# Optimization experiments

Hardware: AMD Instinct MI355X
Metric: run time of the kernel (lower is better)

The kernel has to match this reference:

```python
import jax, jax.numpy as jnp
import numpy as np

B, S, HID = 2, 2048, 1024
HEADS, DHEAD = 16, 64
INNER = HEADS * DHEAD


def setup_inputs() -> dict:
    key = jax.random.key(0)
    ks = jax.random.split(key, 12)
    s = 0.02
    return {
        "query": jax.random.normal(ks[0], (B, S, HID), jnp.float32),
        "key": jax.random.normal(ks[1], (B, S, HID), jnp.float32),
        "value": jax.random.normal(ks[2], (B, S, HID), jnp.float32),
        "mask": jnp.zeros((B, 1, S, S), jnp.float32),
        "position_bias": jax.random.normal(ks[3], (1, HEADS, S, S), jnp.float32),
        "Wq": jax.random.normal(ks[4], (HID, INNER), jnp.float32) * s,
        "bq": jnp.zeros((INNER,), jnp.float32),
        "Wk": jax.random.normal(ks[5], (HID, INNER), jnp.float32) * s,
        "bk": jnp.zeros((INNER,), jnp.float32),
        "Wv": jax.random.normal(ks[6], (HID, INNER), jnp.float32) * s,
        "bv": jnp.zeros((INNER,), jnp.float32),
        "Wo": jax.random.normal(ks[7], (INNER, HID), jnp.float32) * s,
        "bo": jnp.zeros((HID,), jnp.float32),
    }


def reference(query, key, value, mask, position_bias,
              Wq, bq, Wk, bk, Wv, bv, Wo, bo):
    # project and split heads: [B,S,HID] -> [B,HEADS,S,DHEAD]
    def shape(x, W, b):
        return (x @ W + b).reshape(B, S, HEADS, DHEAD).transpose(0, 2, 1, 3)

    q = shape(query, Wq, bq)
    k = shape(key, Wk, bk)
    v = shape(value, Wv, bv)

    scores = jnp.einsum("bhqd,bhkd->bhqk", q, k)
    scores = scores + position_bias          # bias added BEFORE scaling (as in source)
    scores = scores / jnp.sqrt(jnp.float32(DHEAD))
    scores = scores + mask                   # additive mask
    probs = jax.nn.softmax(scores, axis=-1)  # dropout p=0.0 -> identity

    out = jnp.einsum("bhqk,bhkd->bhqd", probs, v)
    out = out.transpose(0, 2, 1, 3).reshape(B, S, INNER)
    return out @ Wo + bo
```

## Files before the change

kernel.cpp:

```cpp
#include <hip/hip_runtime.h>
#include <cstdint>
#include <cstddef>

#define B_SZ      2
#define S_LEN     2048
#define HID_DIM   1024
#define N_HEAD    16
#define D_HEAD    64
#define INNER_DIM 1024

#define C1 0.18033688011112042f
#define C2 1.44269504088896340736f

typedef __attribute__((ext_vector_type(8))) short bf16x8;
typedef __attribute__((ext_vector_type(4))) float f32x4;

__device__ __forceinline__ unsigned short f2bf(float f) {
  unsigned int u = __float_as_uint(f);
  u += 0x7fffu + ((u >> 16) & 1u);
  return (unsigned short)(u >> 16);
}
__device__ __forceinline__ float bf2f(unsigned short u) {
  return __uint_as_float(((unsigned int)u) << 16);
}

__device__ __forceinline__ void gload_lds16(const void* g, void* l) {
  __builtin_amdgcn_global_load_lds((const __attribute__((address_space(1))) void*)g,
                                   (__attribute__((address_space(3))) void*)l,
                                   16, 0, 0);
}

__global__ void cast3_kernel(const float* __restrict__ i0, const float* __restrict__ i1,
                             const float* __restrict__ i2,
                             unsigned short* __restrict__ o0, unsigned short* __restrict__ o1,
                             unsigned short* __restrict__ o2, int n4) {
  int z = blockIdx.y;
  const float* in = (z == 0) ? i0 : (z == 1) ? i1 : i2;
  unsigned short* out = (z == 0) ? o0 : (z == 1) ? o1 : o2;
  int i = blockIdx.x * blockDim.x + threadIdx.x;
  if (i < n4) {
    float4 v = ((const float4*)in)[i];
    ushort4 o;
    o.x = f2bf(v.x); o.y = f2bf(v.y); o.z = f2bf(v.z); o.w = f2bf(v.w);
    ((ushort4*)out)[i] = o;
  }
}

__global__ void transpose_cast_kernel(const float* __restrict__ in,
                                      unsigned short* __restrict__ out,
                                      int rows, int cols) {
  __shared__ float tile[32][33];
  int bx = blockIdx.x * 32;
  int by = blockIdx.y * 32;
  int tx = threadIdx.x & 31;
  int ty = threadIdx.x >> 5;
#pragma unroll
  for (int i = 0; i < 32; i += 8)
    tile[ty + i][tx] = in[(size_t)(by + ty + i) * cols + bx + tx];
  __syncthreads();
#pragma unroll
  for (int i = 0; i < 32; i += 8)
    out[(size_t)(bx + ty + i) * rows + by + tx] = f2bf(tile[tx][ty + i]);
}


__global__ __launch_bounds__(256, 2)
void qkv_gemm_kernel(const unsigned short* __restrict__ Aq,
                     const unsigned short* __restrict__ Ak,
                     const unsigned short* __restrict__ Av,
                     const unsigned short* __restrict__ Wq,
                     const unsigned short* __restrict__ Wk,
                     const unsigned short* __restrict__ Wv,
                     const float* __restrict__ bq,
                     const float* __restrict__ bk,
                     const float* __restrict__ bv,
                     unsigned short* __restrict__ Oq,
                     unsigned short* __restrict__ Ok,
                     unsigned short* __restrict__ Ov) {
  constexpr int K = 1024;
  __shared__ unsigned short Asm[128 * 64];
  __shared__ unsigned short Bsm[64 * 64];

  const int z = blockIdx.z;
  const unsigned short* A  = (z == 0) ? Aq : (z == 1) ? Ak : Av;
  const unsigned short* Bt = (z == 0) ? Wq : (z == 1) ? Wk : Wv;
  const float* bias        = (z == 0) ? bq : (z == 1) ? bk : bv;
  const float scale        = (z == 0) ? C1 : 1.0f;

  const int tid = threadIdx.x;
  const int lane = tid & 63;
  const int w = tid >> 6;
  const int wm = w & 1;
  const int wn = w >> 1;
  const int c = lane & 15;
  const int g = lane >> 4;
  const int m0 = blockIdx.x * 128;
  const int n0 = blockIdx.y * 64;

  f32x4 acc[4][2];
  f32x4 zero = {0.f, 0.f, 0.f, 0.f};
#pragma unroll
  for (int mt = 0; mt < 4; ++mt)
#pragma unroll
    for (int nt = 0; nt < 2; ++nt) acc[mt][nt] = zero;

  for (int kk = 0; kk < K / 64; ++kk) {
    __syncthreads();
    const int k0 = kk * 64;
#pragma unroll
    for (int it = 0; it < 4; ++it) {
      int slot = it * 256 + tid;
      int r = slot >> 3, sp = slot & 7, seg = sp ^ (r & 7);
      gload_lds16(A + (size_t)(m0 + r) * K + k0 + seg * 8,
                  (char*)Asm + (it * 256 + w * 64) * 16);
    }
#pragma unroll
    for (int it = 0; it < 2; ++it) {
      int slot = it * 256 + tid;
      int r = slot >> 3, sp = slot & 7, seg = sp ^ (r & 7);
      gload_lds16(Bt + (size_t)(n0 + r) * K + k0 + seg * 8,
                  (char*)Bsm + (it * 256 + w * 64) * 16);
    }
    __syncthreads();

#pragma unroll
    for (int ks = 0; ks < 2; ++ks) {
      bf16x8 aF[4];
#pragma unroll
      for (int mt = 0; mt < 4; ++mt) {
        int r = wm * 64 + mt * 16 + c;
        int seg = (ks * 4 + g) ^ (r & 7);
        aF[mt] = *(const bf16x8*)((const char*)Asm + r * 128 + seg * 16);
      }
#pragma unroll
      for (int nt = 0; nt < 2; ++nt) {
        int r = wn * 32 + nt * 16 + c;
        int seg = (ks * 4 + g) ^ (r & 7);
        bf16x8 bF = *(const bf16x8*)((const char*)Bsm + r * 128 + seg * 16);
#pragma unroll
        for (int mt = 0; mt < 4; ++mt)
          acc[mt][nt] = __builtin_amdgcn_mfma_f32_16x16x32_bf16(aF[mt], bF, acc[mt][nt], 0, 0, 0);
      }
    }
  }

#pragma unroll
  for (int nt = 0; nt < 2; ++nt) {
    int n_g = n0 + wn * 32 + nt * 16 + c;
    float bvv = bias[n_g];
#pragma unroll
    for (int mt = 0; mt < 4; ++mt) {
      int m_base = m0 + wm * 64 + mt * 16 + g * 4;
      if (z == 2) {
        int b = m_base >> 11;
        int s = m_base & 2047;
        int hh = n_g >> 6;
        int d = n_g & 63;
        ushort4 pk;
        pk.x = f2bf(acc[mt][nt][0] + bvv);
        pk.y = f2bf(acc[mt][nt][1] + bvv);
        pk.z = f2bf(acc[mt][nt][2] + bvv);
        pk.w = f2bf(acc[mt][nt][3] + bvv);
        *(ushort4*)(Ov + ((size_t)((b * N_HEAD + hh) * D_HEAD + d)) * S_LEN + s) = pk;
      } else {
        unsigned short* o = (z == 0) ? Oq : Ok;
#pragma unroll
        for (int r = 0; r < 4; ++r)
          o[(size_t)(m_base + r) * INNER_DIM + n_g] = f2bf((acc[mt][nt][r] + bvv) * scale);
      }
    }
  }
}

__global__ __launch_bounds__(256, 2)
void out_gemm_kernel(const unsigned short* __restrict__ A,
                     const unsigned short* __restrict__ Bt,
                     const float* __restrict__ bias,
                     float* __restrict__ out) {
  constexpr int K = 1024;
  __shared__ unsigned short Asm[128 * 64];
  __shared__ unsigned short Bsm[64 * 64];

  const int tid = threadIdx.x;
  const int lane = tid & 63;
  const int w = tid >> 6;
  const int wm = w & 1;
  const int wn = w >> 1;
  const int c = lane & 15;
  const int g = lane >> 4;
  const int m0 = blockIdx.x * 128;
  const int n0 = blockIdx.y * 64;

  f32x4 acc[4][2];
  f32x4 zero = {0.f, 0.f, 0.f, 0.f};
#pragma unroll
  for (int mt = 0; mt < 4; ++mt)
#pragma unroll
    for (int nt = 0; nt < 2; ++nt) acc[mt][nt] = zero;

  for (int kk = 0; kk < K / 64; ++kk) {
    __syncthreads();
    const int k0 = kk * 64;
#pragma unroll
    for (int it = 0; it < 4; ++it) {
      int slot = it * 256 + tid;
      int r = slot >> 3, sp = slot & 7, seg = sp ^ (r & 7);
      gload_lds16(A + (size_t)(m0 + r) * K + k0 + seg * 8,
                  (char*)Asm + (it * 256 + w * 64) * 16);
    }
#pragma unroll
    for (int it = 0; it < 2; ++it) {
      int slot = it * 256 + tid;
      int r = slot >> 3, sp = slot & 7, seg = sp ^ (r & 7);
      gload_lds16(Bt + (size_t)(n0 + r) * K + k0 + seg * 8,
                  (char*)Bsm + (it * 256 + w * 64) * 16);
    }
    __syncthreads();

#pragma unroll
    for (int ks = 0; ks < 2; ++ks) {
      bf16x8 aF[4];
#pragma unroll
      for (int mt = 0; mt < 4; ++mt) {
        int r = wm * 64 + mt * 16 + c;
        int seg = (ks * 4 + g) ^ (r & 7);
        aF[mt] = *(const bf16x8*)((const char*)Asm + r * 128 + seg * 16);
      }
#pragma unroll
      for (int nt = 0; nt < 2; ++nt) {
        int r = wn * 32 + nt * 16 + c;
        int seg = (ks * 4 + g) ^ (r & 7);
        bf16x8 bF = *(const bf16x8*)((const char*)Bsm + r * 128 + seg * 16);
#pragma unroll
        for (int mt = 0; mt < 4; ++mt)
          acc[mt][nt] = __builtin_amdgcn_mfma_f32_16x16x32_bf16(aF[mt], bF, acc[mt][nt], 0, 0, 0);
      }
    }
  }

#pragma unroll
  for (int nt = 0; nt < 2; ++nt) {
    int n_g = n0 + wn * 32 + nt * 16 + c;
    float bvv = bias[n_g];
#pragma unroll
    for (int mt = 0; mt < 4; ++mt) {
      int m_base = m0 + wm * 64 + mt * 16 + g * 4;
#pragma unroll
      for (int r = 0; r < 4; ++r)
        out[(size_t)(m_base + r) * HID_DIM + n_g] = acc[mt][nt][r] + bvv;
    }
  }
}

__global__ __launch_bounds__(256, 4)
void attn_kernel(const unsigned short* __restrict__ Qp,
                 const unsigned short* __restrict__ Kp,
                 const unsigned short* __restrict__ Vp,
                 const float* __restrict__ bias,
                 const float* __restrict__ mask,
                 unsigned short* __restrict__ Osm) {
  __shared__ unsigned short Ksm0[64 * 64];
  __shared__ unsigned short Ksm1[64 * 64];
  __shared__ unsigned short Vsm0[64 * 64];
  __shared__ unsigned short Vsm1[64 * 64];
  __shared__ unsigned short Psm[64 * 64];

  const int tid = threadIdx.x;
  const int lane = tid & 63;
  const int w = tid >> 6;
  const int c = lane & 15;
  const int g = lane >> 4;
  const int q0 = blockIdx.x * 64;
  const int h = blockIdx.y;
  const int b = blockIdx.z;

  char* Pw = (char*)Psm + w * 2048;

  bf16x8 qF[2];
  {
    size_t row = (size_t)(b * S_LEN + q0 + w * 16 + c);
#pragma unroll
    for (int ks = 0; ks < 2; ++ks)
      qF[ks] = *(const bf16x8*)(Qp + row * INNER_DIM + h * D_HEAD + ks * 32 + g * 8);
  }

  const float* bias_base = bias + ((size_t)h * S_LEN + q0 + w * 16 + g * 4) * S_LEN + c;
  const float* mask_base = mask + ((size_t)b * S_LEN + q0 + w * 16 + g * 4) * S_LEN + c;

  const unsigned short* kSrc[2];
  const unsigned short* vSrc[2];
#pragma unroll
  for (int it = 0; it < 2; ++it) {
    int slot = it * 256 + tid;
    int r = slot >> 3, sp = slot & 7, seg = sp ^ (r & 7);
    kSrc[it] = Kp + (size_t)(b * S_LEN + r) * INNER_DIM + h * D_HEAD + seg * 8;
    vSrc[it] = Vp + ((size_t)((b * N_HEAD + h) * D_HEAD + r)) * S_LEN + seg * 8;
  }

  auto STAGE = [&](int jt, unsigned short* Kd, unsigned short* Vd) {
#pragma unroll
    for (int it = 0; it < 2; ++it)
      gload_lds16(kSrc[it] + (size_t)jt * (64 * INNER_DIM),
                  (char*)Kd + (it * 256 + w * 64) * 16);
#pragma unroll
    for (int it = 0; it < 2; ++it)
      gload_lds16(vSrc[it] + jt * 64,
                  (char*)Vd + (it * 256 + w * 64) * 16);
  };

  float bpre[16], mpre[16];
  auto BM_PRE = [&](int jt) {
#pragma unroll
    for (int nt = 0; nt < 4; ++nt)
#pragma unroll
      for (int r = 0; r < 4; ++r) {
        bpre[nt * 4 + r] = bias_base[(size_t)r * S_LEN + jt * 64 + nt * 16];
        mpre[nt * 4 + r] = mask_base[(size_t)r * S_LEN + jt * 64 + nt * 16];
      }
  };

  float lsum[4];
  f32x4 oacc[4];
  f32x4 zero = {0.f, 0.f, 0.f, 0.f};
#pragma unroll
  for (int r = 0; r < 4; ++r) lsum[r] = 0.f;
#pragma unroll
  for (int dt = 0; dt < 4; ++dt) oacc[dt] = zero;

  STAGE(0, Ksm0, Vsm0);
  BM_PRE(0);

  for (int j = 0; j < S_LEN / 64; ++j) {
    __syncthreads();
    const int pu = j & 1;
    const unsigned short* Kc = pu ? Ksm1 : Ksm0;
    const unsigned short* Vc = pu ? Vsm1 : Vsm0;
    unsigned short* Kn = pu ? Ksm0 : Ksm1;
    unsigned short* Vn = pu ? Vsm0 : Vsm1;
    const int jn = (j + 1 < S_LEN / 64) ? j + 1 : j;

    STAGE(jn, Kn, Vn);

    f32x4 sAcc[4];
#pragma unroll
    for (int nt = 0; nt < 4; ++nt) sAcc[nt] = zero;
#pragma unroll
    for (int ks = 0; ks < 2; ++ks)
#pragma unroll
      for (int nt = 0; nt < 4; ++nt) {
        int r = nt * 16 + c;
        int seg = (ks * 4 + g) ^ (r & 7);
        bf16x8 kF = *(const bf16x8*)((const char*)Kc + r * 128 + seg * 16);
        sAcc[nt] = __builtin_amdgcn_mfma_f32_16x16x32_bf16(qF[ks], kF, sAcc[nt], 0, 0, 0);
      }

#pragma unroll
    for (int r = 0; r < 4; ++r) {
      float pv[4];
#pragma unroll
      for (int nt = 0; nt < 4; ++nt) {
        float t = __builtin_fmaf(bpre[nt * 4 + r], C1,
                  __builtin_fmaf(mpre[nt * 4 + r], C2, sAcc[nt][r]));
        pv[nt] = __builtin_amdgcn_exp2f(t);
        sAcc[nt][r] = pv[nt];
      }
      lsum[r] += (pv[0] + pv[1]) + (pv[2] + pv[3]);
    }

    BM_PRE(jn);

#pragma unroll
    for (int nt = 0; nt < 4; ++nt)
#pragma unroll
      for (int r = 0; r < 4; ++r) {
        int row_l = g * 4 + r;
        int kv = nt * 16 + c;
        int seg = (kv >> 3) ^ (row_l & 7);
        *(unsigned short*)(Pw + row_l * 128 + seg * 16 + (kv & 7) * 2) = f2bf(sAcc[nt][r]);
      }

#pragma unroll
    for (int ks = 0; ks < 2; ++ks) {
      int segP = (ks * 4 + g) ^ (c & 7);
      bf16x8 aP = *(const bf16x8*)(Pw + c * 128 + segP * 16);
#pragma unroll
      for (int dt = 0; dt < 4; ++dt) {
        int dr = dt * 16 + c;
        int segV = (ks * 4 + g) ^ (dr & 7);
        bf16x8 vF = *(const bf16x8*)((const char*)Vc + dr * 128 + segV * 16);
        oacc[dt] = __builtin_amdgcn_mfma_f32_16x16x32_bf16(aP, vF, oacc[dt], 0, 0, 0);
      }
    }
  }

#pragma unroll
  for (int r = 0; r < 4; ++r) {
    float s = lsum[r];
    s += __shfl_xor(s, 1);
    s += __shfl_xor(s, 2);
    s += __shfl_xor(s, 4);
    s += __shfl_xor(s, 8);
    float inv = 1.f / s;
    int qg = q0 + w * 16 + g * 4 + r;
#pragma unroll
    for (int dt = 0; dt < 4; ++dt)
      Osm[(size_t)(b * S_LEN + qg) * INNER_DIM + h * D_HEAD + dt * 16 + c] =
          f2bf(oacc[dt][r] * inv);
  }
}

extern "C" void kernel_launch(void* const* d_in, const int* in_sizes, int n_in,
                              void* d_out, int out_size, void* d_ws, size_t ws_size,
                              hipStream_t stream) {
  const float* query = (const float*)d_in[0];
  const float* key   = (const float*)d_in[1];
  const float* value = (const float*)d_in[2];
  const float* mask  = (const float*)d_in[3];
  const float* bias  = (const float*)d_in[4];
  const float* Wq = (const float*)d_in[5];
  const float* bq = (const float*)d_in[6];
  const float* Wk = (const float*)d_in[7];
  const float* bk = (const float*)d_in[8];
  const float* Wv = (const float*)d_in[9];
  const float* bv = (const float*)d_in[10];
  const float* Wo = (const float*)d_in[11];
  const float* bo = (const float*)d_in[12];

  const size_t NTOK   = (size_t)B_SZ * S_LEN;
  const size_t SZ_ACT = NTOK * INNER_DIM;
  const size_t SZ_W   = (size_t)HID_DIM * INNER_DIM;

  unsigned short* ws  = (unsigned short*)d_ws;
  unsigned short* qb  = ws;
  unsigned short* kb  = qb + SZ_ACT;
  unsigned short* vb  = kb + SZ_ACT;
  unsigned short* Wqt = vb + SZ_ACT;
  unsigned short* Wkt = Wqt + SZ_W;
  unsigned short* Wvt = Wkt + SZ_W;
  unsigned short* Wot = Wvt + SZ_W;
  unsigned short* Qp  = Wot + SZ_W;
  unsigned short* Kp  = Qp + SZ_ACT;
  unsigned short* Vp  = Kp + SZ_ACT;
  unsigned short* Ob  = Vp + SZ_ACT;

  int n4 = (int)(SZ_ACT / 4);
  int cblk = (n4 + 255) / 256;
  dim3 cgrid(cblk, 3);
  cast3_kernel<<<cgrid, 256, 0, stream>>>(query, key, value, qb, kb, vb, n4);

  dim3 tgrid(INNER_DIM / 32, HID_DIM / 32);
  transpose_cast_kernel<<<tgrid, 256, 0, stream>>>(Wq, Wqt, HID_DIM, INNER_DIM);
  transpose_cast_kernel<<<tgrid, 256, 0, stream>>>(Wk, Wkt, HID_DIM, INNER_DIM);
  transpose_cast_kernel<<<tgrid, 256, 0, stream>>>(Wv, Wvt, HID_DIM, INNER_DIM);
  transpose_cast_kernel<<<tgrid, 256, 0, stream>>>(Wo, Wot, INNER_DIM, HID_DIM);

  dim3 ggrid(NTOK / 128, INNER_DIM / 64, 3);
  qkv_gemm_kernel<<<ggrid, 256, 0, stream>>>(qb, kb, vb, Wqt, Wkt, Wvt,
                                             bq, bk, bv, Qp, Kp, Vp);

  dim3 agrid(S_LEN / 64, N_HEAD, B_SZ);
  attn_kernel<<<agrid, 256, 0, stream>>>(Qp, Kp, Vp, bias, mask, Ob);

  dim3 ogrid(NTOK / 128, HID_DIM / 64);
  out_gemm_kernel<<<ogrid, 256, 0, stream>>>(Ob, Wot, bo, (float*)d_out);
}
```

Measured before the change: 578.4 us.

## Share position bias across batches in attention and enlarge GEMM N tiles

The attention kernel now processes both batch elements in one block, so each position_bias tile (a 256MB fp32 tensor shared across batch) is read from global memory once instead of twice. Bias and mask are pre-fused per batch, and K/V staging is doubled to cover both batches, which raises LDS use and register pressure; occupancy drops to 2 blocks per CU. Separately, the QKV and output GEMMs widen their N tile from 64 to 128 for more operand reuse, at the cost of fewer blocks in the grid.

Measured after the change: 570.9 us. Within noise of the previous version (-1.3%).

```diff
diff --git a/kernel.cpp b/kernel.cpp
--- a/kernel.cpp
+++ b/kernel.cpp
@@ -79,7 +79,7 @@
                      unsigned short* __restrict__ Ov) {
   constexpr int K = 1024;
   __shared__ unsigned short Asm[128 * 64];
-  __shared__ unsigned short Bsm[64 * 64];
+  __shared__ unsigned short Bsm[128 * 64];
 
   const int z = blockIdx.z;
   const unsigned short* A  = (z == 0) ? Aq : (z == 1) ? Ak : Av;
@@ -95,14 +95,14 @@
   const int c = lane & 15;
   const int g = lane >> 4;
   const int m0 = blockIdx.x * 128;
-  const int n0 = blockIdx.y * 64;
-
-  f32x4 acc[4][2];
+  const int n0 = blockIdx.y * 128;
+
+  f32x4 acc[4][4];
   f32x4 zero = {0.f, 0.f, 0.f, 0.f};
 #pragma unroll
   for (int mt = 0; mt < 4; ++mt)
 #pragma unroll
-    for (int nt = 0; nt < 2; ++nt) acc[mt][nt] = zero;
+    for (int nt = 0; nt < 4; ++nt) acc[mt][nt] = zero;
 
   for (int kk = 0; kk < K / 64; ++kk) {
     __syncthreads();
@@ -115,7 +115,7 @@
                   (char*)Asm + (it * 256 + w * 64) * 16);
     }
 #pragma unroll
-    for (int it = 0; it < 2; ++it) {
+    for (int it = 0; it < 4; ++it) {
       int slot = it * 256 + tid;
       int r = slot >> 3, sp = slot & 7, seg = sp ^ (r & 7);
       gload_lds16(Bt + (size_t)(n0 + r) * K + k0 + seg * 8,
@@ -133,8 +133,8 @@
         aF[mt] = *(const bf16x8*)((const char*)Asm + r * 128 + seg * 16);
       }
 #pragma unroll
-      for (int nt = 0; nt < 2; ++nt) {
-        int r = wn * 32 + nt * 16 + c;
+      for (int nt = 0; nt < 4; ++nt) {
+        int r = wn * 64 + nt * 16 + c;
         int seg = (ks * 4 + g) ^ (r & 7);
         bf16x8 bF = *(const bf16x8*)((const char*)Bsm + r * 128 + seg * 16);
 #pragma unroll
@@ -145,8 +145,8 @@
   }
 
 #pragma unroll
-  for (int nt = 0; nt < 2; ++nt) {
-    int n_g = n0 + wn * 32 + nt * 16 + c;
+  for (int nt = 0; nt < 4; ++nt) {
+    int n_g = n0 + wn * 64 + nt * 16 + c;
     float bvv = bias[n_g];
 #pragma unroll
     for (int mt = 0; mt < 4; ++mt) {
@@ -179,7 +179,7 @@
                      float* __restrict__ out) {
   constexpr int K = 1024;
   __shared__ unsigned short Asm[128 * 64];
-  __shared__ unsigned short Bsm[64 * 64];
+  __shared__ unsigned short Bsm[128 * 64];
 
   const int tid = threadIdx.x;
   const int lane = tid & 63;
@@ -189,14 +189,14 @@
   const int c = lane & 15;
   const int g = lane >> 4;
   const int m0 = blockIdx.x * 128;
-  const int n0 = blockIdx.y * 64;
-
-  f32x4 acc[4][2];
+  const int n0 = blockIdx.y * 128;
+
+  f32x4 acc[4][4];
   f32x4 zero = {0.f, 0.f, 0.f, 0.f};
 #pragma unroll
   for (int mt = 0; mt < 4; ++mt)
 #pragma unroll
-    for (int nt = 0; nt < 2; ++nt) acc[mt][nt] = zero;
+    for (int nt = 0; nt < 4; ++nt) acc[mt][nt] = zero;
 
   for (int kk = 0; kk < K / 64; ++kk) {
     __syncthreads();
@@ -209,7 +209,7 @@
                   (char*)Asm + (it * 256 + w * 64) * 16);
     }
 #pragma unroll
-    for (int it = 0; it < 2; ++it) {
+    for (int it = 0; it < 4; ++it) {
       int slot = it * 256 + tid;
       int r = slot >> 3, sp = slot & 7, seg = sp ^ (r & 7);
       gload_lds16(Bt + (size_t)(n0 + r) * K + k0 + seg * 8,
@@ -227,8 +227,8 @@
         aF[mt] = *(const bf16x8*)((const char*)Asm + r * 128 + seg * 16);
       }
 #pragma unroll
-      for (int nt = 0; nt < 2; ++nt) {
-        int r = wn * 32 + nt * 16 + c;
+      for (int nt = 0; nt < 4; ++nt) {
+        int r = wn * 64 + nt * 16 + c;
         int seg = (ks * 4 + g) ^ (r & 7);
         bf16x8 bF = *(const bf16x8*)((const char*)Bsm + r * 128 + seg * 16);
 #pragma unroll
@@ -239,8 +239,8 @@
   }
 
 #pragma unroll
-  for (int nt = 0; nt < 2; ++nt) {
-    int n_g = n0 + wn * 32 + nt * 16 + c;
+  for (int nt = 0; nt < 4; ++nt) {
+    int n_g = n0 + wn * 64 + nt * 16 + c;
     float bvv = bias[n_g];
 #pragma unroll
     for (int mt = 0; mt < 4; ++mt) {
@@ -252,17 +252,15 @@
   }
 }
 
-__global__ __launch_bounds__(256, 4)
+__global__ __launch_bounds__(256, 2)
 void attn_kernel(const unsigned short* __restrict__ Qp,
                  const unsigned short* __restrict__ Kp,
                  const unsigned short* __restrict__ Vp,
                  const float* __restrict__ bias,
                  const float* __restrict__ mask,
                  unsigned short* __restrict__ Osm) {
-  __shared__ unsigned short Ksm0[64 * 64];
-  __shared__ unsigned short Ksm1[64 * 64];
-  __shared__ unsigned short Vsm0[64 * 64];
-  __shared__ unsigned short Vsm1[64 * 64];
+  __shared__ unsigned short Ksm[2][2][64 * 64];
+  __shared__ unsigned short Vsm[2][2][64 * 64];
   __shared__ unsigned short Psm[64 * 64];
 
   const int tid = threadIdx.x;
@@ -272,141 +270,154 @@
   const int g = lane >> 4;
   const int q0 = blockIdx.x * 64;
   const int h = blockIdx.y;
-  const int b = blockIdx.z;
 
   char* Pw = (char*)Psm + w * 2048;
 
-  bf16x8 qF[2];
-  {
-    size_t row = (size_t)(b * S_LEN + q0 + w * 16 + c);
+  bf16x8 qF[2][2];
+#pragma unroll
+  for (int bb = 0; bb < 2; ++bb) {
+    size_t row = (size_t)(bb * S_LEN + q0 + w * 16 + c);
 #pragma unroll
     for (int ks = 0; ks < 2; ++ks)
-      qF[ks] = *(const bf16x8*)(Qp + row * INNER_DIM + h * D_HEAD + ks * 32 + g * 8);
-  }
-
-  const float* bias_base = bias + ((size_t)h * S_LEN + q0 + w * 16 + g * 4) * S_LEN + c;
-  const float* mask_base = mask + ((size_t)b * S_LEN + q0 + w * 16 + g * 4) * S_LEN + c;
-
-  const unsigned short* kSrc[2];
-  const unsigned short* vSrc[2];
-#pragma unroll
-  for (int it = 0; it < 2; ++it) {
-    int slot = it * 256 + tid;
-    int r = slot >> 3, sp = slot & 7, seg = sp ^ (r & 7);
-    kSrc[it] = Kp + (size_t)(b * S_LEN + r) * INNER_DIM + h * D_HEAD + seg * 8;
-    vSrc[it] = Vp + ((size_t)((b * N_HEAD + h) * D_HEAD + r)) * S_LEN + seg * 8;
-  }
-
-  auto STAGE = [&](int jt, unsigned short* Kd, unsigned short* Vd) {
-#pragma unroll
-    for (int it = 0; it < 2; ++it)
-      gload_lds16(kSrc[it] + (size_t)jt * (64 * INNER_DIM),
-                  (char*)Kd + (it * 256 + w * 64) * 16);
-#pragma unroll
-    for (int it = 0; it < 2; ++it)
-      gload_lds16(vSrc[it] + jt * 64,
-                  (char*)Vd + (it * 256 + w * 64) * 16);
+      qF[bb][ks] = *(const bf16x8*)(Qp + row * INNER_DIM + h * D_HEAD + ks * 32 + g * 8);
+  }
+
+  const float* bias_base  = bias + ((size_t)h * S_LEN + q0 + w * 16 + g * 4) * S_LEN + c;
+  const float* mask_base0 = mask + ((size_t)(0 * S_LEN) + q0 + w * 16 + g * 4) * S_LEN + c;
+  const float* mask_base1 = mask + ((size_t)(1 * S_LEN) + q0 + w * 16 + g * 4) * S_LEN + c;
+
+  const unsigned short* kSrc[2][2];
+  const unsigned short* vSrc[2][2];
+#pragma unroll
+  for (int bb = 0; bb < 2; ++bb)
+#pragma unroll
+    for (int it = 0; it < 2; ++it) {
+      int slot = it * 256 + tid;
+      int r = slot >> 3, sp = slot & 7, seg = sp ^ (r & 7);
+      kSrc[bb][it] = Kp + (size_t)(bb * S_LEN + r) * INNER_DIM + h * D_HEAD + seg * 8;
+      vSrc[bb][it] = Vp + ((size_t)((bb * N_HEAD + h) * D_HEAD + r)) * S_LEN + seg * 8;
+    }
+
+  auto STAGE = [&](int jt, int pb) {
+#pragma unroll
+    for (int bb = 0; bb < 2; ++bb)
+#pragma unroll
+      for (int it = 0; it < 2; ++it) {
+        gload_lds16(kSrc[bb][it] + (size_t)jt * (64 * INNER_DIM),
+                    (char*)Ksm[pb][bb] + (it * 256 + w * 64) * 16);
+        gload_lds16(vSrc[bb][it] + jt * 64,
+                    (char*)Vsm[pb][bb] + (it * 256 + w * 64) * 16);
+      }
   };
 
-  float bpre[16], mpre[16];
+  float bpre[16], mpre[2][16];
   auto BM_PRE = [&](int jt) {
 #pragma unroll
     for (int nt = 0; nt < 4; ++nt)
 #pragma unroll
       for (int r = 0; r < 4; ++r) {
-        bpre[nt * 4 + r] = bias_base[(size_t)r * S_LEN + jt * 64 + nt * 16];
-        mpre[nt * 4 + r] = mask_base[(size_t)r * S_LEN + jt * 64 + nt * 16];
+        size_t off = (size_t)r * S_LEN + jt * 64 + nt * 16;
+        bpre[nt * 4 + r]    = bias_base[off];
+        mpre[0][nt * 4 + r] = mask_base0[off];
+        mpre[1][nt * 4 + r] = mask_base1[off];
       }
   };
 
-  float lsum[4];
-  f32x4 oacc[4];
+  float lsum[2][4];
+  f32x4 oacc[2][4];
   f32x4 zero = {0.f, 0.f, 0.f, 0.f};
 #pragma unroll
-  for (int r = 0; r < 4; ++r) lsum[r] = 0.f;
-#pragma unroll
-  for (int dt = 0; dt < 4; ++dt) oacc[dt] = zero;
-
-  STAGE(0, Ksm0, Vsm0);
+  for (int bb = 0; bb < 2; ++bb)
+#pragma unroll
+    for (int r = 0; r < 4; ++r) { lsum[bb][r] = 0.f; oacc[bb][r] = zero; }
+
+  STAGE(0, 0);
   BM_PRE(0);
 
   for (int j = 0; j < S_LEN / 64; ++j) {
     __syncthreads();
     const int pu = j & 1;
-    const unsigned short* Kc = pu ? Ksm1 : Ksm0;
-    const unsigned short* Vc = pu ? Vsm1 : Vsm0;
-    unsigned short* Kn = pu ? Ksm0 : Ksm1;
-    unsigned short* Vn = pu ? Vsm0 : Vsm1;
     const int jn = (j + 1 < S_LEN / 64) ? j + 1 : j;
 
-    STAGE(jn, Kn, Vn);
-
-    f32x4 sAcc[4];
-#pragma unroll
-    for (int nt = 0; nt < 4; ++nt) sAcc[nt] = zero;
-#pragma unroll
-    for (int ks = 0; ks < 2; ++ks)
-#pragma unroll
-      for (int nt = 0; nt < 4; ++nt) {
-        int r = nt * 16 + c;
-        int seg = (ks * 4 + g) ^ (r & 7);
-        bf16x8 kF = *(const bf16x8*)((const char*)Kc + r * 128 + seg * 16);
-        sAcc[nt] = __builtin_amdgcn_mfma_f32_16x16x32_bf16(qF[ks], kF, sAcc[nt], 0, 0, 0);
-      }
-
+    STAGE(jn, pu ^ 1);
+
+    float fuse[2][16];
+#pragma unroll
+    for (int i = 0; i < 16; ++i) {
+      float bb_ = bpre[i] * C1;
+      fuse[0][i] = __builtin_fmaf(mpre[0][i], C2, bb_);
+      fuse[1][i] = __builtin_fmaf(mpre[1][i], C2, bb_);
+    }
+    BM_PRE(jn);
+
+#pragma unroll
+    for (int bb = 0; bb < 2; ++bb) {
+      f32x4 sAcc[4];
+#pragma unroll
+      for (int nt = 0; nt < 4; ++nt) sAcc[nt] = zero;
+#pragma unroll
+      for (int ks = 0; ks < 2; ++ks)
+#pragma unroll
+        for (int nt = 0; nt < 4; ++nt) {
+          int r = nt * 16 + c;
+          int seg = (ks * 4 + g) ^ (r & 7);
+          bf16x8 kF = *(const bf16x8*)((const char*)Ksm[pu][bb] + r * 128 + seg * 16);
+          sAcc[nt] = __builtin_amdgcn_mfma_f32_16x16x32_bf16(qF[bb][ks], kF, sAcc[nt], 0, 0, 0);
+        }
+
+#pragma unroll
+      for (int r = 0; r < 4; ++r) {
+        float pv[4];
+#pragma unroll
+        for (int nt = 0; nt < 4; ++nt) {
+          float t = sAcc[nt][r] + fuse[bb][nt * 4 + r];
+          pv[nt] = __builtin_amdgcn_exp2f(t);
+          sAcc[nt][r] = pv[nt];
+        }
+        lsum[bb][r] += (pv[0] + pv[1]) + (pv[2] + pv[3]);
+      }
+
+#pragma unroll
+      for (int nt = 0; nt < 4; ++nt)
+#pragma unroll
+        for (int r = 0; r < 4; ++r) {
+          int row_l = g * 4 + r;
+          int kv = nt * 16 + c;
+          int seg = (kv >> 3) ^ (row_l & 7);
+          *(unsigned short*)(Pw + row_l * 128 + seg * 16 + (kv & 7) * 2) = f2bf(sAcc[nt][r]);
+        }
+
+#pragma unroll
+      for (int ks = 0; ks < 2; ++ks) {
+        int segP = (ks * 4 + g) ^ (c & 7);
+        bf16x8 aP = *(const bf16x8*)(Pw + c * 128 + segP * 16);
+#pragma unroll
+        for (int dt = 0; dt < 4; ++dt) {
+          int dr = dt * 16 + c;
+          int segV = (ks * 4 + g) ^ (dr & 7);
+          bf16x8 vF = *(const bf16x8*)((const char*)Vsm[pu][bb] + dr * 128 + segV * 16);
+          oacc[bb][dt] = __builtin_amdgcn_mfma_f32_16x16x32_bf16(aP, vF, oacc[bb][dt], 0, 0, 0);
+        }
+      }
+    }
+  }
+
+#pragma unroll
+  for (int bb = 0; bb < 2; ++bb)
 #pragma unroll
     for (int r = 0; r < 4; ++r) {
-      float pv[4];
-#pragma unroll
-      for (int nt = 0; nt < 4; ++nt) {
-        float t = __builtin_fmaf(bpre[nt * 4 + r], C1,
-                  __builtin_fmaf(mpre[nt * 4 + r], C2, sAcc[nt][r]));
-        pv[nt] = __builtin_amdgcn_exp2f(t);
-        sAcc[nt][r] = pv[nt];
-      }
-      lsum[r] += (pv[0] + pv[1]) + (pv[2] + pv[3]);
-    }
-
-    BM_PRE(jn);
-
-#pragma unroll
-    for (int nt = 0; nt < 4; ++nt)
-#pragma unroll
-      for (int r = 0; r < 4; ++r) {
-        int row_l = g * 4 + r;
-        int kv = nt * 16 + c;
-        int seg = (kv >> 3) ^ (row_l & 7);
-        *(unsigned short*)(Pw + row_l * 128 + seg * 16 + (kv & 7) * 2) = f2bf(sAcc[nt][r]);
-      }
-
-#pragma unroll
-    for (int ks = 0; ks < 2; ++ks) {
-      int segP = (ks * 4 + g) ^ (c & 7);
-      bf16x8 aP = *(const bf16x8*)(Pw + c * 128 + segP * 16);
-#pragma unroll
-      for (int dt = 0; dt < 4; ++dt) {
-        int dr = dt * 16 + c;
-        int segV = (ks * 4 + g) ^ (dr & 7);
-        bf16x8 vF = *(const bf16x8*)((const char*)Vc + dr * 128 + segV * 16);
-        oacc[dt] = __builtin_amdgcn_mfma_f32_16x16x32_bf16(aP, vF, oacc[dt], 0, 0, 0);
-      }
-    }
-  }
-
-#pragma unroll
-  for (int r = 0; r < 4; ++r) {
-    float s = lsum[r];
-    s += __shfl_xor(s, 1);
-    s += __shfl_xor(s, 2);
-    s += __shfl_xor(s, 4);
-    s += __shfl_xor(s, 8);
-    float inv = 1.f / s;
-    int qg = q0 + w * 16 + g * 4 + r;
-#pragma unroll
-    for (int dt = 0; dt < 4; ++dt)
-      Osm[(size_t)(b * S_LEN + qg) * INNER_DIM + h * D_HEAD + dt * 16 + c] =
-          f2bf(oacc[dt][r] * inv);
-  }
+      float s = lsum[bb][r];
+      s += __shfl_xor(s, 1);
+      s += __shfl_xor(s, 2);
+      s += __shfl_xor(s, 4);
+      s += __shfl_xor(s, 8);
+      float inv = 1.f / s;
+      int qg = q0 + w * 16 + g * 4 + r;
+#pragma unroll
+      for (int dt = 0; dt < 4; ++dt)
+        Osm[(size_t)(bb * S_LEN + qg) * INNER_DIM + h * D_HEAD + dt * 16 + c] =
+            f2bf(oacc[bb][dt][r] * inv);
+    }
 }
 
 extern "C" void kernel_launch(void* const* d_in, const int* in_sizes, int n_in,
@@ -454,13 +465,13 @@
   transpose_cast_kernel<<<tgrid, 256, 0, stream>>>(Wv, Wvt, HID_DIM, INNER_DIM);
   transpose_cast_kernel<<<tgrid, 256, 0, stream>>>(Wo, Wot, INNER_DIM, HID_DIM);
 
-  dim3 ggrid(NTOK / 128, INNER_DIM / 64, 3);
+  dim3 ggrid(NTOK / 128, INNER_DIM / 128, 3);
   qkv_gemm_kernel<<<ggrid, 256, 0, stream>>>(qb, kb, vb, Wqt, Wkt, Wvt,
                                              bq, bk, bv, Qp, Kp, Vp);
 
-  dim3 agrid(S_LEN / 64, N_HEAD, B_SZ);
+  dim3 agrid(S_LEN / 64, N_HEAD);
   attn_kernel<<<agrid, 256, 0, stream>>>(Qp, Kp, Vp, bias, mask, Ob);
 
-  dim3 ogrid(NTOK / 128, HID_DIM / 64);
+  dim3 ogrid(NTOK / 128, HID_DIM / 128);
   out_gemm_kernel<<<ogrid, 256, 0, stream>>>(Ob, Wot, bo, (float*)d_out);
 }
```
